# Performance work log

Hardware: AMD Instinct MI355X
Metric: run time of the kernel (lower is better)

Reference implementation:

```python
import jax, jax.numpy as jnp
import numpy as np

B, C, H, W = 16, 64, 128, 128
C8 = C // 8


def setup_inputs() -> dict:
    key = jax.random.key(0)
    ks = jax.random.split(key, 8)
    s = 0.05
    return {
        "x": jax.random.normal(ks[0], (B, C, H, W), dtype=jnp.float32),
        "Wq": jax.random.normal(ks[1], (C8, C), dtype=jnp.float32) * s,
        "bq": jax.random.normal(ks[2], (C8,), dtype=jnp.float32) * s,
        "Wk": jax.random.normal(ks[3], (C8, C), dtype=jnp.float32) * s,
        "bk": jax.random.normal(ks[4], (C8,), dtype=jnp.float32) * s,
        "Wv": jax.random.normal(ks[5], (C, C), dtype=jnp.float32) * s,
        "bv": jax.random.normal(ks[6], (C,), dtype=jnp.float32) * s,
        "gamma": jnp.zeros((1,), dtype=jnp.float32),
    }


def _criss_cross(x, Wq, bq, Wk, bk, Wv, bv, gamma):
    # 1x1 convs == channel-mixing matmuls
    q = jnp.einsum("bchw,oc->bohw", x, Wq) + bq[None, :, None, None]  # [B,C8,H,W]
    k = jnp.einsum("bchw,oc->bohw", x, Wk) + bk[None, :, None, None]  # [B,C8,H,W]
    v = jnp.einsum("bchw,oc->bohw", x, Wv) + bv[None, :, None, None]  # [B,C,H,W]

    h = x.shape[2]
    # column (H-axis) attention scores; diagonal masked to -inf
    energy_H = jnp.einsum("bchw,bciw->bhwi", q, k)  # [B,H,W,H]
    diag = jnp.eye(h, dtype=bool)[None, :, None, :]  # mask where query row == key row
    energy_H = jnp.where(diag, -jnp.inf, energy_H)
    # row (W-axis) attention scores
    energy_W = jnp.einsum("bchw,bchj->bhwj", q, k)  # [B,H,W,W]

    # joint softmax over concatenated H+W axis
    att = jax.nn.softmax(jnp.concatenate([energy_H, energy_W], axis=3), axis=3)
    att_H = att[:, :, :, :h]    # [B,H,W,H]
    att_W = att[:, :, :, h:]    # [B,H,W,W]

    out_H = jnp.einsum("bhwi,bciw->bchw", att_H, v)
    out_W = jnp.einsum("bhwj,bchj->bchw", att_W, v)
    return gamma[0] * (out_H + out_W) + x


def reference(x, Wq, bq, Wk, bk, Wv, bv, gamma):
    return _criss_cross(x, Wq, bq, Wk, bk, Wv, bv, gamma)
```

## Files before the change

### kernel.cpp

```cpp
#include <hip/hip_runtime.h>

#define HW 128
#define CC 64
#define C8V 8
#define NB 16

typedef _Float16 h1;
typedef _Float16 h2 __attribute__((ext_vector_type(2)));
typedef _Float16 half8 __attribute__((ext_vector_type(8)));
typedef float float16v __attribute__((ext_vector_type(16)));
typedef uint uv4 __attribute__((ext_vector_type(4)));

__device__ __forceinline__ uint packh2(float a, float b) {
#if __has_builtin(__builtin_amdgcn_cvt_pkrtz)
  return __builtin_bit_cast(uint, __builtin_amdgcn_cvt_pkrtz(a, b));
#else
  h2 v; v[0] = (h1)a; v[1] = (h1)b; return __builtin_bit_cast(uint, v);
#endif
}
__device__ __forceinline__ ushort f2h(float a) { h1 v = (h1)a; return __builtin_bit_cast(ushort, v); }
__device__ __forceinline__ float  h2f(ushort a) { return (float)__builtin_bit_cast(h1, a); }

__device__ __forceinline__ float16v mfma16(uv4 a, uv4 b, float16v c) {
  return __builtin_amdgcn_mfma_f32_32x32x16_f16(
      __builtin_bit_cast(half8, a), __builtin_bit_cast(half8, b), c, 0, 0, 0);
}

__global__ __launch_bounds__(256) void k_proj(
    const float* __restrict__ x,
    const float* __restrict__ Wq, const float* __restrict__ bq,
    const float* __restrict__ Wk, const float* __restrict__ bk,
    const float* __restrict__ Wv, const float* __restrict__ bv,
    ushort* __restrict__ q, ushort* __restrict__ k, ushort* __restrict__ v)
{
  alignas(16) __shared__ ushort smem[16128];
  __shared__ float bias_l[96];
  ushort* x_l = smem;
  ushort* W_l = smem + 128 * 72;

  int t = threadIdx.x;
  int lane = t & 63, wv = t >> 6;
  int b = blockIdx.x >> 7, r = blockIdx.x & 127;

  #pragma unroll
  for (int i = 0; i < 20; ++i) {
    int idx = t + 256 * i; int o_ = idx >> 6, c = idx & 63;
    float wval = (o_ < 8) ? Wq[o_ * 64 + c] : (o_ < 16) ? Wk[(o_ - 8) * 64 + c] : Wv[(o_ - 16) * 64 + c];
    W_l[o_ * 72 + c] = f2h(wval);
  }
  if (t < 96) bias_l[t] = (t < 8) ? bq[t] : (t < 16) ? bk[t - 8] : (t < 80) ? bv[t - 16] : 0.f;

  const float* xrow = x + (size_t)(b * CC) * (HW * HW) + (size_t)r * HW;
  #pragma unroll
  for (int i = 0; i < 8; ++i) {
    int idx = t + 256 * i; int c = idx >> 5, w4 = idx & 31;
    float4 xv = *(const float4*)(xrow + (size_t)c * (HW * HW) + w4 * 4);
    x_l[(w4 * 4 + 0) * 72 + c] = f2h(xv.x);
    x_l[(w4 * 4 + 1) * 72 + c] = f2h(xv.y);
    x_l[(w4 * 4 + 2) * 72 + c] = f2h(xv.z);
    x_l[(w4 * 4 + 3) * 72 + c] = f2h(xv.w);
  }
  __syncthreads();

  int w = 32 * wv + (lane & 31);
  float16v acc0 = {}, acc1 = {}, acc2 = {};
  #pragma unroll
  for (int ks = 0; ks < 4; ++ks) {
    int c0 = 8 * (lane >> 5) + 16 * ks;
    uv4 Bx = *(const uv4*)&x_l[w * 72 + c0];
    uv4 a0 = *(const uv4*)&W_l[((lane & 31) + 0) * 72 + c0];
    uv4 a1 = *(const uv4*)&W_l[((lane & 31) + 32) * 72 + c0];
    uv4 a2 = *(const uv4*)&W_l[((lane & 31) + 64) * 72 + c0];
    acc0 = mfma16(a0, Bx, acc0);
    acc1 = mfma16(a1, Bx, acc1);
    acc2 = mfma16(a2, Bx, acc2);
  }
  __syncthreads();

  ushort* o_l = smem;
  int hi = lane >> 5;
  #pragma unroll
  for (int reg = 0; reg < 16; ++reg) {
    int orow = (reg & 3) + 8 * (reg >> 2) + 4 * hi;
    o_l[(orow +  0) * 128 + w] = f2h(acc0[reg] + bias_l[orow]);
    o_l[(orow + 32) * 128 + w] = f2h(acc1[reg] + bias_l[orow + 32]);
    if (orow + 64 < 80)
      o_l[(orow + 64) * 128 + w] = f2h(acc2[reg] + bias_l[orow + 64]);
  }
  __syncthreads();

  ushort* qb = q + (size_t)(b * C8V) * (HW * HW) + (size_t)r * HW;
  ushort* kb = k + (size_t)(b * C8V) * (HW * HW) + (size_t)r * HW;
  ushort* vb = v + (size_t)(b * CC)  * (HW * HW) + (size_t)r * HW;
  #pragma unroll
  for (int i = 0; i < 5; ++i) {
    int idx = t + 256 * i; int o_ = idx >> 4, w8 = idx & 15;
    uv4 val = *(const uv4*)&o_l[o_ * 128 + w8 * 8];
    ushort* dst = (o_ < 8) ? qb + (size_t)o_ * (HW * HW)
                : (o_ < 16) ? kb + (size_t)(o_ - 8) * (HW * HW)
                            : vb + (size_t)(o_ - 16) * (HW * HW);
    *(uv4*)(dst + w8 * 8) = val;
  }
}

__global__ __launch_bounds__(256) void k_transpose_all(
    const ushort* __restrict__ q, ushort* __restrict__ qT,
    const ushort* __restrict__ k, ushort* __restrict__ kT,
    const ushort* __restrict__ v, ushort* __restrict__ vT)
{
  __shared__ ushort tl[128 * 130];
  int t = threadIdx.x;
  int p = blockIdx.x;
  const ushort* in; ushort* out;
  if (p < 128)      { size_t base = (size_t)p * (HW * HW);         in = q + base; out = qT + base; }
  else if (p < 256) { size_t base = (size_t)(p - 128) * (HW * HW); in = k + base; out = kT + base; }
  else              { size_t base = (size_t)(p - 256) * (HW * HW); in = v + base; out = vT + base; }
  const uint* ip = (const uint*)in;
  uint* op = (uint*)out;
  int c2 = t & 63;
  int r0 = t >> 6;
  for (int it = 0; it < 32; ++it) {
    int r = it * 4 + r0;
    uint val = ip[r * 64 + c2];
    *(uint*)&tl[r * 130 + c2 * 2] = val;
  }
  __syncthreads();
  for (int it = 0; it < 32; ++it) {
    int wcol = it * 4 + r0;
    int hh = c2 * 2;
    uint lo = tl[hh * 130 + wcol];
    uint hi = tl[(hh + 1) * 130 + wcol];
    op[wcol * 64 + c2] = lo | (hi << 16);
  }
}

template<bool MASK>
__global__ __launch_bounds__(256) void k_attn(
    const ushort* __restrict__ q, const ushort* __restrict__ kk, const ushort* __restrict__ v,
    ushort* __restrict__ o, float* __restrict__ m_out, float* __restrict__ s_out)
{
  alignas(16) __shared__ ushort Q_l[128][16];
  alignas(16) __shared__ ushort K_l[128][16];
  alignas(16) __shared__ uint   V_l[64 * 64];

  int t = threadIdx.x;
  int lane = t & 63, wv = t >> 6;
  int hi = lane >> 5;
  int b = blockIdx.x >> 7, r = blockIdx.x & 127;
  size_t plane32 = (size_t)(HW * HW) / 2;

  if (t < 128) {
    *(uv4*)&Q_l[t][8] = (uv4){0, 0, 0, 0};
    *(uv4*)&K_l[t][8] = (uv4){0, 0, 0, 0};
  }
  const uint* qrow = (const uint*)q + (size_t)(b * C8V) * plane32 + (size_t)r * 64;
  const uint* krow = (const uint*)kk + (size_t)(b * C8V) * plane32 + (size_t)r * 64;
  #pragma unroll
  for (int i = 0; i < 2; ++i) {
    int idx = t + 256 * i; int c = idx >> 6, w2 = idx & 63;
    uint qv = qrow[(size_t)c * plane32 + w2];
    Q_l[2 * w2][c] = (ushort)(qv & 0xffff); Q_l[2 * w2 + 1][c] = (ushort)(qv >> 16);
    uint kv = krow[(size_t)c * plane32 + w2];
    K_l[2 * w2][c] = (ushort)(kv & 0xffff); K_l[2 * w2 + 1][c] = (ushort)(kv >> 16);
  }
  const uint* vrow = (const uint*)v + (size_t)(b * CC) * plane32 + (size_t)r * 64;
  #pragma unroll
  for (int i = 0; i < 16; ++i) {
    int idx = t + 256 * i; int c = idx >> 6, j2 = idx & 63;
    uint val = vrow[(size_t)c * plane32 + j2];
    uint byteoff = c * 256 + ((4 * j2) ^ ((c & 15) << 4));
    V_l[byteoff >> 2] = val;
  }
  __syncthreads();

  uv4 Bq = *(const uv4*)&Q_l[(lane & 31) + 32 * wv][hi * 8];
  float16v e[4];
  #pragma unroll
  for (int mt = 0; mt < 4; ++mt) {
    uv4 ka = *(const uv4*)&K_l[(lane & 31) + 32 * mt][hi * 8];
    float16v z = {};
    e[mt] = mfma16(ka, Bq, z);
  }

  int qg = 32 * wv + (lane & 31);
  float m = -INFINITY;
  #pragma unroll
  for (int mt = 0; mt < 4; ++mt) {
    #pragma unroll
    for (int reg = 0; reg < 16; ++reg) {
      float ev = e[mt][reg];
      if (MASK) {
        int key = 32 * mt + ((reg & 3) + 8 * (reg >> 2) + 4 * hi);
        ev = (key == qg) ? -INFINITY : ev;
        e[mt][reg] = ev;
      }
      m = fmaxf(m, ev);
    }
  }
  m = fmaxf(m, __shfl_xor(m, 32));
  float s = 0.f;
  #pragma unroll
  for (int mt = 0; mt < 4; ++mt) {
    #pragma unroll
    for (int reg = 0; reg < 16; ++reg) {
      float p = __expf(e[mt][reg] - m);
      e[mt][reg] = p;
      s += p;
    }
  }
  s += __shfl_xor(s, 32);
  if (lane < 32) {
    m_out[(size_t)blockIdx.x * HW + qg] = m;
    s_out[(size_t)blockIdx.x * HW + qg] = s;
  }

  float16v acc0 = {}, acc1 = {};
  #pragma unroll
  for (int s8 = 0; s8 < 8; ++s8) {
    int mt = s8 >> 1, hf = s8 & 1;
    float p0 = e[mt][8 * hf + 0], p1 = e[mt][8 * hf + 1];
    float p2 = e[mt][8 * hf + 2], p3 = e[mt][8 * hf + 3];
    float p4 = e[mt][8 * hf + 4], p5 = e[mt][8 * hf + 5];
    float p6 = e[mt][8 * hf + 6], p7 = e[mt][8 * hf + 7];
    uint X = packh2(p0, p1), Y = packh2(p2, p3), Z = packh2(p4, p5), Wp = packh2(p6, p7);
    uint Xs = __shfl_xor(X, 32), Ys = __shfl_xor(Y, 32);
    uint Zs = __shfl_xor(Z, 32), Ws = __shfl_xor(Wp, 32);
    uv4 Bp;
    Bp[0] = (hi == 0) ? X  : Zs;
    Bp[1] = (hi == 0) ? Y  : Ws;
    Bp[2] = (hi == 0) ? Xs : Z;
    Bp[3] = (hi == 0) ? Ys : Wp;
    #pragma unroll
    for (int ct = 0; ct < 2; ++ct) {
      int c = (lane & 31) + 32 * ct;
      uint byteoff = c * 256 + ((16 * (hi + 2 * s8)) ^ ((c & 15) << 4));
      uv4 va = *(const uv4*)((const char*)V_l + byteoff);
      if (ct == 0) acc0 = mfma16(va, Bp, acc0);
      else         acc1 = mfma16(va, Bp, acc1);
    }
  }

  __syncthreads();
  ushort* o_l = (ushort*)V_l;
  int w = 32 * wv + (lane & 31);
  #pragma unroll
  for (int reg = 0; reg < 16; ++reg) {
    int c = (reg & 3) + 8 * (reg >> 2) + 4 * hi;
    o_l[(c +  0) * 128 + w] = f2h(acc0[reg]);
    o_l[(c + 32) * 128 + w] = f2h(acc1[reg]);
  }
  __syncthreads();
  ushort* ob = o + (size_t)(b * CC) * (HW * HW) + (size_t)r * HW;
  #pragma unroll
  for (int i = 0; i < 4; ++i) {
    int idx = t + 256 * i; int c = idx >> 4, w8 = idx & 15;
    *(uv4*)(ob + (size_t)c * (HW * HW) + w8 * 8) = *(const uv4*)&o_l[c * 128 + w8 * 8];
  }
}

__global__ __launch_bounds__(256) void k_merge(
    const ushort* __restrict__ oHT, const ushort* __restrict__ oW,
    const float* __restrict__ mH, const float* __restrict__ sH,
    const float* __restrict__ mW, const float* __restrict__ sW,
    const float* __restrict__ x, const float* __restrict__ gamma,
    float* __restrict__ out)
{
  __shared__ float aH_l[32 * 132];
  __shared__ float aW_l[128 * 33];
  __shared__ float tile[32 * 132];

  int t = threadIdx.x;
  int bid = blockIdx.x;
  int wsel = bid & 3;
  int cg = (bid >> 2) & 7;
  int b = bid >> 5;
  int w0 = wsel * 32;
  float g = gamma[0];
  const int PL = HW * HW;

  #pragma unroll
  for (int it = 0; it < 16; ++it) {
    int p = t + 256 * it;
    int w = p & 31, h = p >> 5;
    float mw = mW[b * PL + h * HW + w0 + w];
    float sw = sW[b * PL + h * HW + w0 + w];
    float mh = mH[b * PL + (w0 + w) * HW + h];
    float sh = sH[b * PL + (w0 + w) * HW + h];
    float mm = fmaxf(mh, mw);
    float eh = __expf(mh - mm), ew = __expf(mw - mm);
    float inv = 1.f / (sh * eh + sw * ew);
    aH_l[w * 132 + h] = eh * inv;
    aW_l[h * 33 + w] = ew * inv;
  }
  __syncthreads();

  for (int ci = 0; ci < 8; ++ci) {
    int c = cg * 8 + ci;
    size_t cbase = (size_t)(b * CC + c) * PL;
    #pragma unroll
    for (int i = 0; i < 2; ++i) {
      int p = t + 256 * i;
      int w = p >> 4, hg = p & 15;
      uv4 ov = *(const uv4*)(oHT + cbase + (size_t)(w0 + w) * HW + hg * 8);
      float* trow = &tile[w * 132 + hg * 8];
      const float* arow = &aH_l[w * 132 + hg * 8];
      #pragma unroll
      for (int j = 0; j < 8; ++j) {
        ushort u = (ushort)((ov[j >> 1] >> ((j & 1) * 16)) & 0xffff);
        trow[j] = h2f(u) * arow[j];
      }
    }
    __syncthreads();
    #pragma unroll
    for (int it = 0; it < 4; ++it) {
      int p = t + 256 * it;
      int w4 = p & 7, h = p >> 3;
      size_t base = cbase + (size_t)h * HW + w0 + 4 * w4;
      uint2 ow2 = *(const uint2*)(oW + base);
      float4 xv = *(const float4*)(x + base);
      const float* aw = &aW_l[h * 33 + 4 * w4];
      float r[4];
      #pragma unroll
      for (int j = 0; j < 4; ++j) {
        ushort u = (ushort)(((j < 2 ? ow2.x : ow2.y) >> ((j & 1) * 16)) & 0xffff);
        float th = tile[(4 * w4 + j) * 132 + h];
        r[j] = g * (th + h2f(u) * aw[j]);
      }
      float4 res = { r[0] + xv.x, r[1] + xv.y, r[2] + xv.z, r[3] + xv.w };
      *(float4*)(out + base) = res;
    }
    __syncthreads();
  }
}

extern "C" void kernel_launch(void* const* d_in, const int* in_sizes, int n_in,
                              void* d_out, int out_size, void* d_ws, size_t ws_size,
                              hipStream_t stream)
{
  const float* x     = (const float*)d_in[0];
  const float* Wq    = (const float*)d_in[1];
  const float* bq    = (const float*)d_in[2];
  const float* Wk    = (const float*)d_in[3];
  const float* bk    = (const float*)d_in[4];
  const float* Wv    = (const float*)d_in[5];
  const float* bv    = (const float*)d_in[6];
  const float* gamma = (const float*)d_in[7];
  float* out = (float*)d_out;

  char* w = (char*)d_ws;
  size_t np = (size_t)NB * HW * HW;
  ushort* q   = (ushort*)w;  w += np * C8V * 2;
  ushort* k   = (ushort*)w;  w += np * C8V * 2;
  ushort* qT  = (ushort*)w;  w += np * C8V * 2;
  ushort* kT  = (ushort*)w;  w += np * C8V * 2;
  ushort* v   = (ushort*)w;  w += np * CC * 2;
  ushort* vT  = (ushort*)w;  w += np * CC * 2;
  ushort* oW  = (ushort*)w;  w += np * CC * 2;
  ushort* oHT = (ushort*)w;  w += np * CC * 2;
  float* mW = (float*)w;  w += np * 4;
  float* sW = (float*)w;  w += np * 4;
  float* mH = (float*)w;  w += np * 4;
  float* sH = (float*)w;  w += np * 4;
  if ((size_t)(w - (char*)d_ws) > ws_size) return;

  k_proj<<<NB * HW, 256, 0, stream>>>(x, Wq, bq, Wk, bk, Wv, bv, q, k, v);
  k_transpose_all<<<256 + NB * CC, 256, 0, stream>>>(q, qT, k, kT, v, vT);
  k_attn<false><<<NB * HW, 256, 0, stream>>>(q,  k,  v,  oW,  mW, sW);
  k_attn<true ><<<NB * HW, 256, 0, stream>>>(qT, kT, vT, oHT, mH, sH);
  k_merge<<<NB * 32, 256, 0, stream>>>(oHT, oW, mH, sH, mW, sW, x, gamma, out);
}
```

Measured before the change: 128.5 us.

## Merge row and column attention launches and restructure merge kernel tiling

The two templated attention launches become one launch over twice the blocks, with the mask selected at runtime from the block index. This removes one kernel launch and the tail gap between the two grids. The merge kernel now runs twice as many blocks, each covering 4 channels instead of 8. It stages the transposed H-side max/sum through shared memory so the global reads are coalesced, and keeps the scaled H output tile in fp16 so the per-channel barriers go away. The cost is a runtime mask branch in the attention kernel and an extra fp16 rounding of the intermediate H term.

```diff
diff --git a/kernel.cpp b/kernel.cpp
--- a/kernel.cpp
+++ b/kernel.cpp
@@ -134,10 +134,11 @@
   }
 }
 
-template<bool MASK>
-__global__ __launch_bounds__(256) void k_attn(
-    const ushort* __restrict__ q, const ushort* __restrict__ kk, const ushort* __restrict__ v,
-    ushort* __restrict__ o, float* __restrict__ m_out, float* __restrict__ s_out)
+__global__ __launch_bounds__(256) void k_attn_both(
+    const ushort* __restrict__ q,  const ushort* __restrict__ kkn, const ushort* __restrict__ vn,
+    const ushort* __restrict__ qT, const ushort* __restrict__ kkT, const ushort* __restrict__ vT,
+    ushort* __restrict__ oW_, float* __restrict__ mW_, float* __restrict__ sW_,
+    ushort* __restrict__ oH_, float* __restrict__ mH_, float* __restrict__ sH_)
 {
   alignas(16) __shared__ ushort Q_l[128][16];
   alignas(16) __shared__ ushort K_l[128][16];
@@ -146,15 +147,24 @@
   int t = threadIdx.x;
   int lane = t & 63, wv = t >> 6;
   int hi = lane >> 5;
-  int b = blockIdx.x >> 7, r = blockIdx.x & 127;
+  int bid = blockIdx.x & 2047;
+  bool maskf = blockIdx.x >= 2048;
+  const ushort* qp = maskf ? qT : q;
+  const ushort* kp = maskf ? kkT : kkn;
+  const ushort* vp = maskf ? vT : vn;
+  ushort* op = maskf ? oH_ : oW_;
+  float* mo = maskf ? mH_ : mW_;
+  float* so = maskf ? sH_ : sW_;
+
+  int b = bid >> 7, r = bid & 127;
   size_t plane32 = (size_t)(HW * HW) / 2;
 
   if (t < 128) {
     *(uv4*)&Q_l[t][8] = (uv4){0, 0, 0, 0};
     *(uv4*)&K_l[t][8] = (uv4){0, 0, 0, 0};
   }
-  const uint* qrow = (const uint*)q + (size_t)(b * C8V) * plane32 + (size_t)r * 64;
-  const uint* krow = (const uint*)kk + (size_t)(b * C8V) * plane32 + (size_t)r * 64;
+  const uint* qrow = (const uint*)qp + (size_t)(b * C8V) * plane32 + (size_t)r * 64;
+  const uint* krow = (const uint*)kp + (size_t)(b * C8V) * plane32 + (size_t)r * 64;
   #pragma unroll
   for (int i = 0; i < 2; ++i) {
     int idx = t + 256 * i; int c = idx >> 6, w2 = idx & 63;
@@ -163,7 +173,7 @@
     uint kv = krow[(size_t)c * plane32 + w2];
     K_l[2 * w2][c] = (ushort)(kv & 0xffff); K_l[2 * w2 + 1][c] = (ushort)(kv >> 16);
   }
-  const uint* vrow = (const uint*)v + (size_t)(b * CC) * plane32 + (size_t)r * 64;
+  const uint* vrow = (const uint*)vp + (size_t)(b * CC) * plane32 + (size_t)r * 64;
   #pragma unroll
   for (int i = 0; i < 16; ++i) {
     int idx = t + 256 * i; int c = idx >> 6, j2 = idx & 63;
@@ -189,7 +199,7 @@
     #pragma unroll
     for (int reg = 0; reg < 16; ++reg) {
       float ev = e[mt][reg];
-      if (MASK) {
+      if (maskf) {
         int key = 32 * mt + ((reg & 3) + 8 * (reg >> 2) + 4 * hi);
         ev = (key == qg) ? -INFINITY : ev;
         e[mt][reg] = ev;
@@ -210,8 +220,8 @@
   }
   s += __shfl_xor(s, 32);
   if (lane < 32) {
-    m_out[(size_t)blockIdx.x * HW + qg] = m;
-    s_out[(size_t)blockIdx.x * HW + qg] = s;
+    mo[(size_t)bid * HW + qg] = m;
+    so[(size_t)bid * HW + qg] = s;
   }
 
   float16v acc0 = {}, acc1 = {};
@@ -250,7 +260,7 @@
     o_l[(c + 32) * 128 + w] = f2h(acc1[reg]);
   }
   __syncthreads();
-  ushort* ob = o + (size_t)(b * CC) * (HW * HW) + (size_t)r * HW;
+  ushort* ob = op + (size_t)(b * CC) * (HW * HW) + (size_t)r * HW;
   #pragma unroll
   for (int i = 0; i < 4; ++i) {
     int idx = t + 256 * i; int c = idx >> 4, w8 = idx & 15;
@@ -265,71 +275,95 @@
     const float* __restrict__ x, const float* __restrict__ gamma,
     float* __restrict__ out)
 {
-  __shared__ float aH_l[32 * 132];
-  __shared__ float aW_l[128 * 33];
-  __shared__ float tile[32 * 132];
+  __shared__ float aH_l[32 * 129];
+  __shared__ float aW_l[128 * 36];
+  alignas(16) __shared__ ushort otile[4 * 32 * 132];
+  float* tmpM = (float*)otile;
+  float* tmpS = tmpM + 32 * 129;
 
   int t = threadIdx.x;
   int bid = blockIdx.x;
-  int wsel = bid & 3;
-  int cg = (bid >> 2) & 7;
-  int b = bid >> 5;
+  int wsel = bid & 3, cg = (bid >> 2) & 15, b = bid >> 6;
   int w0 = wsel * 32;
   float g = gamma[0];
   const int PL = HW * HW;
-
-  #pragma unroll
-  for (int it = 0; it < 16; ++it) {
-    int p = t + 256 * it;
-    int w = p & 31, h = p >> 5;
-    float mw = mW[b * PL + h * HW + w0 + w];
-    float sw = sW[b * PL + h * HW + w0 + w];
-    float mh = mH[b * PL + (w0 + w) * HW + h];
-    float sh = sH[b * PL + (w0 + w) * HW + h];
+  const float* mHb = mH + (size_t)b * PL;
+  const float* sHb = sH + (size_t)b * PL;
+  const float* mWb = mW + (size_t)b * PL;
+  const float* sWb = sW + (size_t)b * PL;
+
+  #pragma unroll
+  for (int i = 0; i < 16; ++i) {
+    int p = t + 256 * i; int h = p & 127, w = p >> 7;
+    tmpM[w * 129 + h] = mHb[(w0 + w) * HW + h];
+    tmpS[w * 129 + h] = sHb[(w0 + w) * HW + h];
+  }
+  __syncthreads();
+  #pragma unroll
+  for (int i = 0; i < 16; ++i) {
+    int p = t + 256 * i; int w = p & 31, h = p >> 5;
+    float mw = mWb[h * HW + w0 + w], sw = sWb[h * HW + w0 + w];
+    float mh = tmpM[w * 129 + h],    sh = tmpS[w * 129 + h];
     float mm = fmaxf(mh, mw);
     float eh = __expf(mh - mm), ew = __expf(mw - mm);
     float inv = 1.f / (sh * eh + sw * ew);
-    aH_l[w * 132 + h] = eh * inv;
-    aW_l[h * 33 + w] = ew * inv;
-  }
-  __syncthreads();
-
-  for (int ci = 0; ci < 8; ++ci) {
-    int c = cg * 8 + ci;
-    size_t cbase = (size_t)(b * CC + c) * PL;
+    aH_l[w * 129 + h] = eh * inv;
+    aW_l[h * 36 + w]  = ew * inv;
+  }
+  __syncthreads();
+
+  #pragma unroll
+  for (int i = 0; i < 8; ++i) {
+    int p = t + 256 * i;
+    int ch = p >> 9, rest = p & 511;
+    int w = rest >> 4, hg = rest & 15;
+    size_t cbase = (size_t)(b * CC + cg * 4 + ch) * PL;
+    uv4 ov = *(const uv4*)(oHT + cbase + (size_t)(w0 + w) * HW + hg * 8);
+    const float* ah = &aH_l[w * 129 + hg * 8];
+    uint res[4];
+    #pragma unroll
+    for (int jj = 0; jj < 4; ++jj) {
+      float lo = h2f((ushort)(ov[jj] & 0xffff)) * ah[2 * jj];
+      float hi = h2f((ushort)(ov[jj] >> 16))    * ah[2 * jj + 1];
+      res[jj] = packh2(lo, hi);
+    }
+    ushort* dst = &otile[(ch * 32 + w) * 132 + hg * 8];
+    *(uint2*)dst       = make_uint2(res[0], res[1]);
+    *(uint2*)(dst + 4) = make_uint2(res[2], res[3]);
+  }
+  __syncthreads();
+
+  #pragma unroll
+  for (int ch = 0; ch < 4; ++ch) {
+    size_t cbase = (size_t)(b * CC + cg * 4 + ch) * PL;
+    const ushort* otc = &otile[ch * 32 * 132];
     #pragma unroll
     for (int i = 0; i < 2; ++i) {
       int p = t + 256 * i;
-      int w = p >> 4, hg = p & 15;
-      uv4 ov = *(const uv4*)(oHT + cbase + (size_t)(w0 + w) * HW + hg * 8);
-      float* trow = &tile[w * 132 + hg * 8];
-      const float* arow = &aH_l[w * 132 + hg * 8];
+      int w4 = p & 7, h2 = p >> 3;
+      float th0[4], th1[4];
       #pragma unroll
-      for (int j = 0; j < 8; ++j) {
-        ushort u = (ushort)((ov[j >> 1] >> ((j & 1) * 16)) & 0xffff);
-        trow[j] = h2f(u) * arow[j];
+      for (int j = 0; j < 4; ++j) {
+        uint pk = *(const uint*)&otc[(4 * w4 + j) * 132 + 2 * h2];
+        th0[j] = h2f((ushort)(pk & 0xffff));
+        th1[j] = h2f((ushort)(pk >> 16));
+      }
+      #pragma unroll
+      for (int rr = 0; rr < 2; ++rr) {
+        int hh = 2 * h2 + rr;
+        const float* th = rr ? th1 : th0;
+        size_t base = cbase + (size_t)hh * HW + w0 + 4 * w4;
+        float4 aw = *(const float4*)&aW_l[hh * 36 + 4 * w4];
+        uint2 ow2 = *(const uint2*)(oW + base);
+        float4 xv = *(const float4*)(x + base);
+        float4 res;
+        res.x = g * (th[0] + h2f((ushort)(ow2.x & 0xffff)) * aw.x) + xv.x;
+        res.y = g * (th[1] + h2f((ushort)(ow2.x >> 16))    * aw.y) + xv.y;
+        res.z = g * (th[2] + h2f((ushort)(ow2.y & 0xffff)) * aw.z) + xv.z;
+        res.w = g * (th[3] + h2f((ushort)(ow2.y >> 16))    * aw.w) + xv.w;
+        *(float4*)(out + base) = res;
       }
     }
-    __syncthreads();
-    #pragma unroll
-    for (int it = 0; it < 4; ++it) {
-      int p = t + 256 * it;
-      int w4 = p & 7, h = p >> 3;
-      size_t base = cbase + (size_t)h * HW + w0 + 4 * w4;
-      uint2 ow2 = *(const uint2*)(oW + base);
-      float4 xv = *(const float4*)(x + base);
-      const float* aw = &aW_l[h * 33 + 4 * w4];
-      float r[4];
-      #pragma unroll
-      for (int j = 0; j < 4; ++j) {
-        ushort u = (ushort)(((j < 2 ? ow2.x : ow2.y) >> ((j & 1) * 16)) & 0xffff);
-        float th = tile[(4 * w4 + j) * 132 + h];
-        r[j] = g * (th + h2f(u) * aw[j]);
-      }
-      float4 res = { r[0] + xv.x, r[1] + xv.y, r[2] + xv.z, r[3] + xv.w };
-      *(float4*)(out + base) = res;
-    }
-    __syncthreads();
   }
 }
 
@@ -365,7 +399,7 @@
 
   k_proj<<<NB * HW, 256, 0, stream>>>(x, Wq, bq, Wk, bk, Wv, bv, q, k, v);
   k_transpose_all<<<256 + NB * CC, 256, 0, stream>>>(q, qT, k, kT, v, vT);
-  k_attn<false><<<NB * HW, 256, 0, stream>>>(q,  k,  v,  oW,  mW, sW);
-  k_attn<true ><<<NB * HW, 256, 0, stream>>>(qT, kT, vT, oHT, mH, sH);
-  k_merge<<<NB * 32, 256, 0, stream>>>(oHT, oW, mH, sH, mW, sW, x, gamma, out);
-}
+  k_attn_both<<<2 * NB * HW, 256, 0, stream>>>(q, k, v, qT, kT, vT,
+                                               oW, mW, sW, oHT, mH, sH);
+  k_merge<<<NB * 16 * 4, 256, 0, stream>>>(oHT, oW, mH, sH, mW, sW, x, gamma, out);
+}
```

Result: faster. 123.9 us (-3.6%).
